# Kernel optimization log

Measured on AMD Instinct MI355X. Metric: run time of the kernel, lower is better.

## Reference

```python
import jax, jax.numpy as jnp
import numpy as np

N_NODES = 250000


def _glorot(key, shape):
    fan_in, fan_out = shape[0], shape[1]
    lim = jnp.sqrt(6.0 / (fan_in + fan_out))
    return jax.random.uniform(key, shape, jnp.float32, -lim, lim)


def setup_inputs() -> dict:
    key = jax.random.key(0)
    ks = jax.random.split(key, 16)
    x = jax.random.normal(ks[0], (N_NODES, 9), jnp.float32)
    edge_index = jax.random.randint(ks[1], (2, 5000000), 0, N_NODES, jnp.int64)
    return {
        "x": x,
        "edge_index": edge_index,
        "W1": _glorot(ks[2], (9, 16)),  "b1": jnp.zeros((16,), jnp.float32),
        "W2": _glorot(ks[3], (16, 16)), "b2": jnp.zeros((16,), jnp.float32),
        "W3": _glorot(ks[4], (16, 16)), "b3": jnp.zeros((16,), jnp.float32),
        "Wl2": _glorot(ks[5], (25, 128)),  "bl2": jnp.zeros((128,), jnp.float32),
        "Wl3": _glorot(ks[6], (128, 128)), "bl3": jnp.zeros((128,), jnp.float32),
        "Wl4": _glorot(ks[7], (128, 1)),   "bl4": jnp.zeros((1,), jnp.float32),
    }


def _gcn_conv(x, src, dst, norm, W, b, n):
    # PyG GCNConv: linear transform, then D^-1/2 (A+I) D^-1/2 aggregation, then bias
    h = x @ W                                   # [N, d_out]
    msg = h[src] * norm[:, None]                # gather + scale   [E+N, d_out]
    agg = jax.ops.segment_sum(msg, dst, num_segments=n)
    return agg + b


def _sym_norm(src, dst, n):
    deg = jax.ops.segment_sum(jnp.ones_like(dst, jnp.float32), dst, num_segments=n)
    dinv = jnp.where(deg > 0, jax.lax.rsqrt(deg), 0.0)
    return dinv[src] * dinv[dst]


def reference(x, edge_index, W1, b1, W2, b2, W3, b3, Wl2, bl2, Wl3, bl3, Wl4, bl4):
    n = x.shape[0]
    loops = jnp.arange(n, dtype=edge_index.dtype)
    src = jnp.concatenate([edge_index[0], loops])  # add self loops
    dst = jnp.concatenate([edge_index[1], loops])
    norm = _sym_norm(src, dst, n)  # same graph for all 3 conv layers

    h = jax.nn.relu(_gcn_conv(x, src, dst, norm, W1, b1, n))
    h = jax.nn.relu(_gcn_conv(h, src, dst, norm, W2, b2, n))
    h = jax.nn.relu(_gcn_conv(h, src, dst, norm, W3, b3, n))

    h = jnp.concatenate([x, h], axis=1)          # [N, 25]
    h = jax.nn.relu(h @ Wl2 + bl2)
    h = jax.nn.relu(h @ Wl3 + bl3)
    return h @ Wl4 + bl4                         # [N, 1]
```

## Files before the change

kernel.cpp:

```cpp
#include <hip/hip_runtime.h>


#define NBLK 512
#define BSH  9
#define BSZ  512
#define MAXNB 1024

__global__ __launch_bounds__(64) void k_detect(const void* __restrict__ edges,
                                               int* __restrict__ flag, int n_nodes)
{
    if (threadIdx.x == 0 && blockIdx.x == 0) {
        const long long* p = (const long long*)edges;
        int is64 = 1;
        for (int i = 0; i < 16; ++i) {
            long long v = p[i];
            if (v < 0 || v >= (long long)n_nodes) is64 = 0;
        }
        *flag = is64;
    }
}

__device__ __forceinline__ int ld_idx(const void* edges, int f64, long long idx)
{
    return f64 ? ((const int*)edges)[idx << 1] : ((const int*)edges)[idx];
}

__global__ __launch_bounds__(256) void k_hist2(const void* __restrict__ edges,
                                               const int* __restrict__ flag,
                                               int* __restrict__ cnt_blk,
                                               long long E, int NB)
{
    __shared__ int cnt[MAXNB];
    int tid = threadIdx.x;
    for (int b = tid; b < NB; b += 256) cnt[b] = 0;
    __syncthreads();
    int f64 = *flag;
    long long chunk = (E + NBLK - 1) / NBLK;
    long long lo = (long long)blockIdx.x * chunk;
    long long hi = lo + chunk; if (hi > E) hi = E;
    for (long long i = lo + tid; i < hi; i += 256) {
        int d = ld_idx(edges, f64, E + i);
        atomicAdd(&cnt[d >> BSH], 1);
    }
    __syncthreads();
    for (int b = tid; b < NB; b += 256)
        cnt_blk[(size_t)b * NBLK + blockIdx.x] = (cnt[b] + 15) & ~15;
}

__global__ __launch_bounds__(256) void k_scan1(const int* __restrict__ in,
                                               int* __restrict__ excl,
                                               int* __restrict__ partials, int n)
{
    __shared__ int s[256];
    int tid = threadIdx.x;
    int i = blockIdx.x * 256 + tid;
    int v = (i < n) ? in[i] : 0;
    s[tid] = v;
    __syncthreads();
#pragma unroll
    for (int off = 1; off < 256; off <<= 1) {
        int t = (tid >= off) ? s[tid - off] : 0;
        __syncthreads();
        s[tid] += t;
        __syncthreads();
    }
    if (i < n) excl[i] = s[tid] - v;
    if (tid == 255) partials[blockIdx.x] = s[255];
}

__global__ __launch_bounds__(1024) void k_scan2(int* __restrict__ p, int nb)
{
    __shared__ int s[1024];
    __shared__ int carry_s;
    int t = threadIdx.x;
    if (t == 0) carry_s = 0;
    __syncthreads();
    for (int base = 0; base < nb; base += 1024) {
        int idx = base + t;
        int v = (idx < nb) ? p[idx] : 0;
        s[t] = v;
        __syncthreads();
        for (int off = 1; off < 1024; off <<= 1) {
            int u = (t >= off) ? s[t - off] : 0;
            __syncthreads();
            s[t] += u;
            __syncthreads();
        }
        int carry = carry_s;
        if (idx < nb) p[idx] = carry + s[t] - v;
        __syncthreads();
        if (t == 0) carry_s += s[1023];
        __syncthreads();
    }
}

__global__ __launch_bounds__(256) void k_scan3(int* __restrict__ excl,
                                               const int* __restrict__ partials, int n)
{
    int i = blockIdx.x * 256 + threadIdx.x;
    if (i < n) excl[i] += partials[blockIdx.x];
}

__global__ __launch_bounds__(256) void k_bin(const void* __restrict__ edges,
                                             const int* __restrict__ flag,
                                             const int* __restrict__ base_blk,
                                             int* __restrict__ epk,
                                             long long E, int NB)
{
    __shared__ int cnt[MAXNB];
    __shared__ int base[MAXNB];
    __shared__ int cur[MAXNB];
    int tid = threadIdx.x;
    for (int b = tid; b < NB; b += 256) cnt[b] = 0;
    __syncthreads();
    int f64 = *flag;
    long long chunk = (E + NBLK - 1) / NBLK;
    long long lo = (long long)blockIdx.x * chunk;
    long long hi = lo + chunk; if (hi > E) hi = E;
    for (long long i = lo + tid; i < hi; i += 256) {
        int d = ld_idx(edges, f64, E + i);
        atomicAdd(&cnt[d >> BSH], 1);
    }
    __syncthreads();
    for (int b = tid; b < NB; b += 256) {
        base[b] = base_blk[(size_t)b * NBLK + blockIdx.x];
        cur[b] = 0;
    }
    __syncthreads();
    for (long long i = lo + tid; i < hi; i += 256) {
        int s = ld_idx(edges, f64, i);
        int d = ld_idx(edges, f64, E + i);
        int b = d >> BSH;
        int slot = atomicAdd(&cur[b], 1);
        epk[base[b] + slot] = ((d & (BSZ - 1)) << 18) | s;
    }
    __syncthreads();
    for (int b = tid; b < NB; b += 256) {
        int c = cnt[b];
        int r = (c + 15) & ~15;
        for (int j = c; j < r; ++j) epk[base[b] + j] = -1;
    }
}

__global__ __launch_bounds__(256) void k_csr(const int* __restrict__ epk,
                                             const int* __restrict__ base_blk,
                                             int* __restrict__ csr,
                                             int* __restrict__ row_off,
                                             int* __restrict__ degi,
                                             float* __restrict__ dinv, int n)
{
    __shared__ int cnt[BSZ];
    __shared__ int off[BSZ];
    __shared__ int ps[256];
    int b = blockIdx.x;
    int tid = threadIdx.x;
    int start = base_blk[(size_t)b * NBLK];
    int end   = base_blk[(size_t)(b + 1) * NBLK];
    cnt[tid] = 0; cnt[tid + 256] = 0;
    __syncthreads();
    for (int e = start + tid; e < end; e += 256) {
        int pk = epk[e];
        if (pk >= 0) atomicAdd(&cnt[pk >> 18], 1);
    }
    __syncthreads();
    int pairSum = cnt[2 * tid] + cnt[2 * tid + 1];
    ps[tid] = pairSum;
    __syncthreads();
#pragma unroll
    for (int o = 1; o < 256; o <<= 1) {
        int v = (tid >= o) ? ps[tid - o] : 0;
        __syncthreads();
        ps[tid] += v;
        __syncthreads();
    }
    int incl = ps[tid];
    off[2 * tid]     = incl - pairSum;
    off[2 * tid + 1] = incl - pairSum + cnt[2 * tid];
    __syncthreads();
    int nbase = b << BSH;
#pragma unroll
    for (int l = tid; l < BSZ; l += 256) {
        int node = nbase + l;
        if (node < n) {
            row_off[node] = start + off[l];
            degi[node]    = cnt[l];
            dinv[node]    = rsqrtf((float)cnt[l] + 1.0f);
        }
    }
    __syncthreads();
    for (int e = start + tid; e < end; e += 256) {
        int pk = epk[e];
        if (pk < 0) continue;
        int l = pk >> 18;
        int pos = atomicAdd(&off[l], 1);
        csr[start + pos] = pk & 0x3FFFF;
    }
}

__global__ __launch_bounds__(256) void k_lin1(const float* __restrict__ x,
                                              const float* __restrict__ W1,
                                              const float* __restrict__ dinv,
                                              float* __restrict__ hs, int n)
{
    __shared__ float sW[144];
    if (threadIdx.x < 144) sW[threadIdx.x] = W1[threadIdx.x];
    __syncthreads();
    int i = blockIdx.x * 256 + threadIdx.x;
    if (i >= n) return;
    float xv[9];
#pragma unroll
    for (int k = 0; k < 9; ++k) xv[k] = x[(size_t)i * 9 + k];
    float di = dinv[i];
#pragma unroll
    for (int j = 0; j < 16; ++j) {
        float acc = 0.f;
#pragma unroll
        for (int k = 0; k < 9; ++k) acc = fmaf(xv[k], sW[k * 16 + j], acc);
        hs[(size_t)i * 16 + j] = acc * di;
    }
}

__global__ __launch_bounds__(256) void k_lin_mid(const float* __restrict__ bias,
                                                 const float* __restrict__ W,
                                                 const float* __restrict__ dinv,
                                                 const float* __restrict__ agg,
                                                 float* __restrict__ hs, int n)
{
    __shared__ float sW[256];
    __shared__ float sB[16];
    sW[threadIdx.x] = W[threadIdx.x];
    if (threadIdx.x < 16) sB[threadIdx.x] = bias[threadIdx.x];
    __syncthreads();
    int i = blockIdx.x * 256 + threadIdx.x;
    if (i >= n) return;
    float t[16];
#pragma unroll
    for (int k = 0; k < 16; ++k) {
        float v = agg[(size_t)i * 16 + k] + sB[k];
        t[k] = v > 0.f ? v : 0.f;
    }
    float di = dinv[i];
#pragma unroll
    for (int j = 0; j < 16; ++j) {
        float acc = 0.f;
#pragma unroll
        for (int k = 0; k < 16; ++k) acc = fmaf(t[k], sW[k * 16 + j], acc);
        hs[(size_t)i * 16 + j] = acc * di;
    }
}

__global__ __launch_bounds__(256) void k_gather(const int* __restrict__ csr,
                                                const int* __restrict__ row_off,
                                                const int* __restrict__ degi,
                                                const float* __restrict__ dinv,
                                                const float* __restrict__ hs,
                                                float* __restrict__ agg, int n)
{
    int wid = (int)(((long long)blockIdx.x * 256 + threadIdx.x) >> 6);
    if (wid >= n) return;
    int lane = threadIdx.x & 63;
    int slot = lane >> 2;
    int q    = lane & 3;
    int start = row_off[wid];
    int deg   = degi[wid];
    float4 sum;
    if (slot == 0) sum = *(const float4*)&hs[(size_t)wid * 16 + q * 4];
    else           sum = make_float4(0.f, 0.f, 0.f, 0.f);
    for (int e = slot; e < deg; e += 16) {
        int s = csr[start + e];
        float4 v = *(const float4*)&hs[(size_t)s * 16 + q * 4];
        sum.x += v.x; sum.y += v.y; sum.z += v.z; sum.w += v.w;
    }
#pragma unroll
    for (int off = 4; off < 64; off <<= 1) {
        sum.x += __shfl_xor(sum.x, off);
        sum.y += __shfl_xor(sum.y, off);
        sum.z += __shfl_xor(sum.z, off);
        sum.w += __shfl_xor(sum.w, off);
    }
    if (slot == 0) {
        float di = dinv[wid];
        sum.x *= di; sum.y *= di; sum.z *= di; sum.w *= di;
        *(float4*)&agg[(size_t)wid * 16 + q * 4] = sum;
    }
}

__global__ __launch_bounds__(256) void k_mlp(const float* __restrict__ x,
                                             const float* __restrict__ agg3,
                                             const float* __restrict__ b3,
                                             const float* __restrict__ Wl2,
                                             const float* __restrict__ bl2,
                                             const float* __restrict__ Wl3,
                                             const float* __restrict__ bl3,
                                             const float* __restrict__ Wl4,
                                             const float* __restrict__ bl4,
                                             float* __restrict__ out, int n)
{
    __shared__ __align__(16) float zs[4][16][132];
    __shared__ __align__(16) float sfeat[4][16][28];

    int tid  = threadIdx.x;
    int w    = tid >> 6;
    int lane = tid & 63;
    int og   = lane & 15;
    int ng   = lane >> 4;
    int base = (blockIdx.x * 4 + w) * 16;

    for (int idx = lane; idx < 16 * 25; idx += 64) {
        int nn = idx / 25, f = idx - nn * 25;
        int node = base + nn;
        float v = 0.f;
        if (node < n) {
            if (f < 9) v = x[(size_t)node * 9 + f];
            else {
                float t = agg3[(size_t)node * 16 + (f - 9)] + b3[f - 9];
                v = t > 0.f ? t : 0.f;
            }
        }
        sfeat[w][nn][f] = v;
    }
    __syncthreads();

    float acc[4][8];
    {
        float4 b0 = *(const float4*)&bl2[og * 8];
        float4 b1 = *(const float4*)&bl2[og * 8 + 4];
#pragma unroll
        for (int i = 0; i < 4; ++i) {
            acc[i][0] = b0.x; acc[i][1] = b0.y; acc[i][2] = b0.z; acc[i][3] = b0.w;
            acc[i][4] = b1.x; acc[i][5] = b1.y; acc[i][6] = b1.z; acc[i][7] = b1.w;
        }
    }
#pragma unroll
    for (int k = 0; k < 25; ++k) {
        float4 w0 = *(const float4*)&Wl2[k * 128 + og * 8];
        float4 w1 = *(const float4*)&Wl2[k * 128 + og * 8 + 4];
#pragma unroll
        for (int i = 0; i < 4; ++i) {
            float f = sfeat[w][ng * 4 + i][k];
            acc[i][0] = fmaf(f, w0.x, acc[i][0]); acc[i][1] = fmaf(f, w0.y, acc[i][1]);
            acc[i][2] = fmaf(f, w0.z, acc[i][2]); acc[i][3] = fmaf(f, w0.w, acc[i][3]);
            acc[i][4] = fmaf(f, w1.x, acc[i][4]); acc[i][5] = fmaf(f, w1.y, acc[i][5]);
            acc[i][6] = fmaf(f, w1.z, acc[i][6]); acc[i][7] = fmaf(f, w1.w, acc[i][7]);
        }
    }
#pragma unroll
    for (int i = 0; i < 4; ++i) {
        float4 lo, hi;
        lo.x = acc[i][0] > 0.f ? acc[i][0] : 0.f; lo.y = acc[i][1] > 0.f ? acc[i][1] : 0.f;
        lo.z = acc[i][2] > 0.f ? acc[i][2] : 0.f; lo.w = acc[i][3] > 0.f ? acc[i][3] : 0.f;
        hi.x = acc[i][4] > 0.f ? acc[i][4] : 0.f; hi.y = acc[i][5] > 0.f ? acc[i][5] : 0.f;
        hi.z = acc[i][6] > 0.f ? acc[i][6] : 0.f; hi.w = acc[i][7] > 0.f ? acc[i][7] : 0.f;
        *(float4*)&zs[w][ng * 4 + i][og * 8]     = lo;
        *(float4*)&zs[w][ng * 4 + i][og * 8 + 4] = hi;
    }
    __syncthreads();

    {
        float4 b0 = *(const float4*)&bl3[og * 8];
        float4 b1 = *(const float4*)&bl3[og * 8 + 4];
#pragma unroll
        for (int i = 0; i < 4; ++i) {
            acc[i][0] = b0.x; acc[i][1] = b0.y; acc[i][2] = b0.z; acc[i][3] = b0.w;
            acc[i][4] = b1.x; acc[i][5] = b1.y; acc[i][6] = b1.z; acc[i][7] = b1.w;
        }
    }
#pragma unroll 2
    for (int k4 = 0; k4 < 64; k4 += 4) {
        float4 z4[4];
#pragma unroll
        for (int i = 0; i < 4; ++i)
            z4[i] = *(const float4*)&zs[w][ng * 4 + i][k4];
#pragma unroll
        for (int kk = 0; kk < 4; ++kk) {
            const float* wr = &Wl3[(k4 + kk) * 128 + og * 8];
            float4 w0 = *(const float4*)wr;
            float4 w1 = *(const float4*)(wr + 4);
#pragma unroll
            for (int i = 0; i < 4; ++i) {
                float zz = (kk == 0) ? z4[i].x : (kk == 1) ? z4[i].y
                         : (kk == 2) ? z4[i].z : z4[i].w;
                acc[i][0] = fmaf(zz, w0.x, acc[i][0]); acc[i][1] = fmaf(zz, w0.y, acc[i][1]);
                acc[i][2] = fmaf(zz, w0.z, acc[i][2]); acc[i][3] = fmaf(zz, w0.w, acc[i][3]);
                acc[i][4] = fmaf(zz, w1.x, acc[i][4]); acc[i][5] = fmaf(zz, w1.y, acc[i][5]);
                acc[i][6] = fmaf(zz, w1.z, acc[i][6]); acc[i][7] = fmaf(zz, w1.w, acc[i][7]);
            }
        }
    }
    __syncthreads();
#pragma unroll 2
    for (int k4 = 64; k4 < 128; k4 += 4) {
        float4 z4[4];
#pragma unroll
        for (int i = 0; i < 4; ++i)
            z4[i] = *(const float4*)&zs[w][ng * 4 + i][k4];
#pragma unroll
        for (int kk = 0; kk < 4; ++kk) {
            const float* wr = &Wl3[(k4 + kk) * 128 + og * 8];
            float4 w0 = *(const float4*)wr;
            float4 w1 = *(const float4*)(wr + 4);
#pragma unroll
            for (int i = 0; i < 4; ++i) {
                float zz = (kk == 0) ? z4[i].x : (kk == 1) ? z4[i].y
                         : (kk == 2) ? z4[i].z : z4[i].w;
                acc[i][0] = fmaf(zz, w0.x, acc[i][0]); acc[i][1] = fmaf(zz, w0.y, acc[i][1]);
                acc[i][2] = fmaf(zz, w0.z, acc[i][2]); acc[i][3] = fmaf(zz, w0.w, acc[i][3]);
                acc[i][4] = fmaf(zz, w1.x, acc[i][4]); acc[i][5] = fmaf(zz, w1.y, acc[i][5]);
                acc[i][6] = fmaf(zz, w1.z, acc[i][6]); acc[i][7] = fmaf(zz, w1.w, acc[i][7]);
            }
        }
    }

    {
        float4 w40 = *(const float4*)&Wl4[og * 8];
        float4 w41 = *(const float4*)&Wl4[og * 8 + 4];
        float bb = bl4[0];
#pragma unroll
        for (int i = 0; i < 4; ++i) {
            float p = 0.f;
            p = fmaf(acc[i][0] > 0.f ? acc[i][0] : 0.f, w40.x, p);
            p = fmaf(acc[i][1] > 0.f ? acc[i][1] : 0.f, w40.y, p);
            p = fmaf(acc[i][2] > 0.f ? acc[i][2] : 0.f, w40.z, p);
            p = fmaf(acc[i][3] > 0.f ? acc[i][3] : 0.f, w40.w, p);
            p = fmaf(acc[i][4] > 0.f ? acc[i][4] : 0.f, w41.x, p);
            p = fmaf(acc[i][5] > 0.f ? acc[i][5] : 0.f, w41.y, p);
            p = fmaf(acc[i][6] > 0.f ? acc[i][6] : 0.f, w41.z, p);
            p = fmaf(acc[i][7] > 0.f ? acc[i][7] : 0.f, w41.w, p);
            p += __shfl_xor(p, 1);
            p += __shfl_xor(p, 2);
            p += __shfl_xor(p, 4);
            p += __shfl_xor(p, 8);
            int node = base + ng * 4 + i;
            if (og == 0 && node < n) out[node] = p + bb;
        }
    }
}

extern "C" void kernel_launch(void* const* d_in, const int* in_sizes, int n_in,
                              void* d_out, int out_size, void* d_ws, size_t ws_size,
                              hipStream_t stream)
{
    const float* x   = (const float*)d_in[0];
    const void*  ei  = d_in[1];
    const float* W1  = (const float*)d_in[2];
    const float* b1  = (const float*)d_in[3];
    const float* W2  = (const float*)d_in[4];
    const float* b2  = (const float*)d_in[5];
    const float* W3  = (const float*)d_in[6];
    const float* b3  = (const float*)d_in[7];
    const float* Wl2 = (const float*)d_in[8];
    const float* bl2 = (const float*)d_in[9];
    const float* Wl3 = (const float*)d_in[10];
    const float* bl3 = (const float*)d_in[11];
    const float* Wl4 = (const float*)d_in[12];
    const float* bl4 = (const float*)d_in[13];
    float* out = (float*)d_out;

    int n        = in_sizes[0] / 9;
    long long e2 = (long long)in_sizes[1];
    long long E  = e2 / 2;
    int NB       = (n + BSZ - 1) >> BSH;
    int L        = NB * NBLK + 1;
    size_t EPAD  = (size_t)E + (size_t)NBLK * NB * 16;

    char* ws = (char*)d_ws;
    size_t off = 0;
    int*   flag     = (int*)(ws + off); off += 256;
    int*   cnt_blk  = (int*)(ws + off); off += (size_t)L * 4;        off = (off + 255) & ~(size_t)255;
    int*   base_blk = (int*)(ws + off); off += (size_t)L * 4;        off = (off + 255) & ~(size_t)255;
    int*   partials = (int*)(ws + off); off += 16384;
    float* dinv     = (float*)(ws + off); off += (size_t)n * 4;      off = (off + 255) & ~(size_t)255;
    int*   degi     = (int*)(ws + off); off += (size_t)n * 4;        off = (off + 255) & ~(size_t)255;
    int*   row_off  = (int*)(ws + off); off += (size_t)n * 4;        off = (off + 255) & ~(size_t)255;
    int*   csr      = (int*)(ws + off); off += EPAD * 4;             off = (off + 255) & ~(size_t)255;
    int*   epk      = (int*)(ws + off); off += EPAD * 4;             off = (off + 255) & ~(size_t)255;
    float* hs  = (float*)epk;
    float* agg = hs + (size_t)n * 16;

    int nb_n = (n + 255) / 256;
    int nb_s = (L + 255) / 256;

    k_detect<<<1, 64, 0, stream>>>(ei, flag, n);
    hipMemsetAsync(cnt_blk + (L - 1), 0, 4, stream);
    k_hist2<<<NBLK, 256, 0, stream>>>(ei, flag, cnt_blk, E, NB);
    k_scan1<<<nb_s, 256, 0, stream>>>(cnt_blk, base_blk, partials, L);
    k_scan2<<<1, 1024, 0, stream>>>(partials, nb_s);
    k_scan3<<<nb_s, 256, 0, stream>>>(base_blk, partials, L);
    k_bin<<<NBLK, 256, 0, stream>>>(ei, flag, base_blk, epk, E, NB);
    k_csr<<<NB, 256, 0, stream>>>(epk, base_blk, csr, row_off, degi, dinv, n);

    int nb_g = (n + 3) / 4;
    k_lin1<<<nb_n, 256, 0, stream>>>(x, W1, dinv, hs, n);
    k_gather<<<nb_g, 256, 0, stream>>>(csr, row_off, degi, dinv, hs, agg, n);
    k_lin_mid<<<nb_n, 256, 0, stream>>>(b1, W2, dinv, agg, hs, n);
    k_gather<<<nb_g, 256, 0, stream>>>(csr, row_off, degi, dinv, hs, agg, n);
    k_lin_mid<<<nb_n, 256, 0, stream>>>(b2, W3, dinv, agg, hs, n);
    k_gather<<<nb_g, 256, 0, stream>>>(csr, row_off, degi, dinv, hs, agg, n);
    k_mlp<<<(n + 63) / 64, 256, 0, stream>>>(x, agg, b3, Wl2, bl2, Wl3, bl3, Wl4, bl4,
                                             out, n);
}
```

Measured before the change: 602.7 us.

## Fuse GCN linear transform into gather kernel and swizzle MLP shared memory

Merges the per-node 16x16 linear transform (bias, ReLU, matmul, dinv scale) into the neighbor-gather kernel, so the two middle k_lin_mid launches and their round trip of the aggregate buffer through global memory go away. Gather and transform now ping-pong between two buffers. The gather loop is unrolled by two to keep more independent loads in flight. The MLP kernel reuses one shared buffer for both input features and hidden activations, and uses an XOR swizzle instead of padding to avoid bank conflicts, which lowers shared memory use but adds an extra barrier.

```diff
diff --git a/kernel.cpp b/kernel.cpp
--- a/kernel.cpp
+++ b/kernel.cpp
@@ -220,41 +220,15 @@
     }
 }
 
-__global__ __launch_bounds__(256) void k_lin_mid(const float* __restrict__ bias,
+template<int MODE>
+__global__ __launch_bounds__(256) void k_gatherF(const int* __restrict__ csr,
+                                                 const int* __restrict__ row_off,
+                                                 const int* __restrict__ degi,
+                                                 const float* __restrict__ dinv,
+                                                 const float* __restrict__ hs,
                                                  const float* __restrict__ W,
-                                                 const float* __restrict__ dinv,
-                                                 const float* __restrict__ agg,
-                                                 float* __restrict__ hs, int n)
-{
-    __shared__ float sW[256];
-    __shared__ float sB[16];
-    sW[threadIdx.x] = W[threadIdx.x];
-    if (threadIdx.x < 16) sB[threadIdx.x] = bias[threadIdx.x];
-    __syncthreads();
-    int i = blockIdx.x * 256 + threadIdx.x;
-    if (i >= n) return;
-    float t[16];
-#pragma unroll
-    for (int k = 0; k < 16; ++k) {
-        float v = agg[(size_t)i * 16 + k] + sB[k];
-        t[k] = v > 0.f ? v : 0.f;
-    }
-    float di = dinv[i];
-#pragma unroll
-    for (int j = 0; j < 16; ++j) {
-        float acc = 0.f;
-#pragma unroll
-        for (int k = 0; k < 16; ++k) acc = fmaf(t[k], sW[k * 16 + j], acc);
-        hs[(size_t)i * 16 + j] = acc * di;
-    }
-}
-
-__global__ __launch_bounds__(256) void k_gather(const int* __restrict__ csr,
-                                                const int* __restrict__ row_off,
-                                                const int* __restrict__ degi,
-                                                const float* __restrict__ dinv,
-                                                const float* __restrict__ hs,
-                                                float* __restrict__ agg, int n)
+                                                 const float* __restrict__ bias,
+                                                 float* __restrict__ outb, int n)
 {
     int wid = (int)(((long long)blockIdx.x * 256 + threadIdx.x) >> 6);
     if (wid >= n) return;
@@ -263,13 +237,23 @@
     int q    = lane & 3;
     int start = row_off[wid];
     int deg   = degi[wid];
+    float di  = dinv[wid];
     float4 sum;
     if (slot == 0) sum = *(const float4*)&hs[(size_t)wid * 16 + q * 4];
     else           sum = make_float4(0.f, 0.f, 0.f, 0.f);
-    for (int e = slot; e < deg; e += 16) {
-        int s = csr[start + e];
-        float4 v = *(const float4*)&hs[(size_t)s * 16 + q * 4];
-        sum.x += v.x; sum.y += v.y; sum.z += v.z; sum.w += v.w;
+    int e = slot;
+    for (; e + 16 < deg; e += 32) {
+        int s0 = csr[start + e];
+        int s1 = csr[start + e + 16];
+        float4 v0 = *(const float4*)&hs[(size_t)s0 * 16 + q * 4];
+        float4 v1 = *(const float4*)&hs[(size_t)s1 * 16 + q * 4];
+        sum.x += v0.x + v1.x; sum.y += v0.y + v1.y;
+        sum.z += v0.z + v1.z; sum.w += v0.w + v1.w;
+    }
+    if (e < deg) {
+        int s0 = csr[start + e];
+        float4 v0 = *(const float4*)&hs[(size_t)s0 * 16 + q * 4];
+        sum.x += v0.x; sum.y += v0.y; sum.z += v0.z; sum.w += v0.w;
     }
 #pragma unroll
     for (int off = 4; off < 64; off <<= 1) {
@@ -278,10 +262,30 @@
         sum.z += __shfl_xor(sum.z, off);
         sum.w += __shfl_xor(sum.w, off);
     }
-    if (slot == 0) {
-        float di = dinv[wid];
-        sum.x *= di; sum.y *= di; sum.z *= di; sum.w *= di;
-        *(float4*)&agg[(size_t)wid * 16 + q * 4] = sum;
+    float4 aq = make_float4(sum.x * di, sum.y * di, sum.z * di, sum.w * di);
+
+    if (MODE == 0) {
+        if (slot == 0) *(float4*)&outb[(size_t)wid * 16 + q * 4] = aq;
+    } else {
+        float t[16];
+#pragma unroll
+        for (int a = 0; a < 4; ++a) {
+            t[4 * a + 0] = __shfl(aq.x, a);
+            t[4 * a + 1] = __shfl(aq.y, a);
+            t[4 * a + 2] = __shfl(aq.z, a);
+            t[4 * a + 3] = __shfl(aq.w, a);
+        }
+#pragma unroll
+        for (int k = 0; k < 16; ++k) {
+            float v = t[k] + bias[k];
+            t[k] = v > 0.f ? v : 0.f;
+        }
+        int j = lane & 15;
+        float o = 0.f;
+#pragma unroll
+        for (int k = 0; k < 16; ++k)
+            o = fmaf(t[k], W[k * 16 + j], o);
+        if (lane < 16) outb[(size_t)wid * 16 + j] = o * di;
     }
 }
 
@@ -296,8 +300,7 @@
                                              const float* __restrict__ bl4,
                                              float* __restrict__ out, int n)
 {
-    __shared__ __align__(16) float zs[4][16][132];
-    __shared__ __align__(16) float sfeat[4][16][28];
+    __shared__ __align__(16) float zs[4][16][128];
 
     int tid  = threadIdx.x;
     int w    = tid >> 6;
@@ -317,7 +320,7 @@
                 v = t > 0.f ? t : 0.f;
             }
         }
-        sfeat[w][nn][f] = v;
+        zs[w][nn][f] = v;
     }
     __syncthreads();
 
@@ -337,22 +340,26 @@
         float4 w1 = *(const float4*)&Wl2[k * 128 + og * 8 + 4];
 #pragma unroll
         for (int i = 0; i < 4; ++i) {
-            float f = sfeat[w][ng * 4 + i][k];
+            float f = zs[w][ng * 4 + i][k];
             acc[i][0] = fmaf(f, w0.x, acc[i][0]); acc[i][1] = fmaf(f, w0.y, acc[i][1]);
             acc[i][2] = fmaf(f, w0.z, acc[i][2]); acc[i][3] = fmaf(f, w0.w, acc[i][3]);
             acc[i][4] = fmaf(f, w1.x, acc[i][4]); acc[i][5] = fmaf(f, w1.y, acc[i][5]);
             acc[i][6] = fmaf(f, w1.z, acc[i][6]); acc[i][7] = fmaf(f, w1.w, acc[i][7]);
         }
     }
-#pragma unroll
-    for (int i = 0; i < 4; ++i) {
-        float4 lo, hi;
-        lo.x = acc[i][0] > 0.f ? acc[i][0] : 0.f; lo.y = acc[i][1] > 0.f ? acc[i][1] : 0.f;
-        lo.z = acc[i][2] > 0.f ? acc[i][2] : 0.f; lo.w = acc[i][3] > 0.f ? acc[i][3] : 0.f;
-        hi.x = acc[i][4] > 0.f ? acc[i][4] : 0.f; hi.y = acc[i][5] > 0.f ? acc[i][5] : 0.f;
-        hi.z = acc[i][6] > 0.f ? acc[i][6] : 0.f; hi.w = acc[i][7] > 0.f ? acc[i][7] : 0.f;
-        *(float4*)&zs[w][ng * 4 + i][og * 8]     = lo;
-        *(float4*)&zs[w][ng * 4 + i][og * 8 + 4] = hi;
+    __syncthreads();
+    {
+        int c0 = (og * 8) ^ (ng << 3);
+#pragma unroll
+        for (int i = 0; i < 4; ++i) {
+            float4 lo, hi;
+            lo.x = acc[i][0] > 0.f ? acc[i][0] : 0.f; lo.y = acc[i][1] > 0.f ? acc[i][1] : 0.f;
+            lo.z = acc[i][2] > 0.f ? acc[i][2] : 0.f; lo.w = acc[i][3] > 0.f ? acc[i][3] : 0.f;
+            hi.x = acc[i][4] > 0.f ? acc[i][4] : 0.f; hi.y = acc[i][5] > 0.f ? acc[i][5] : 0.f;
+            hi.z = acc[i][6] > 0.f ? acc[i][6] : 0.f; hi.w = acc[i][7] > 0.f ? acc[i][7] : 0.f;
+            *(float4*)&zs[w][ng * 4 + i][c0]     = lo;
+            *(float4*)&zs[w][ng * 4 + i][c0 + 4] = hi;
+        }
     }
     __syncthreads();
 
@@ -365,12 +372,13 @@
             acc[i][4] = b1.x; acc[i][5] = b1.y; acc[i][6] = b1.z; acc[i][7] = b1.w;
         }
     }
+    int swz = ng << 3;
 #pragma unroll 2
     for (int k4 = 0; k4 < 64; k4 += 4) {
         float4 z4[4];
 #pragma unroll
         for (int i = 0; i < 4; ++i)
-            z4[i] = *(const float4*)&zs[w][ng * 4 + i][k4];
+            z4[i] = *(const float4*)&zs[w][ng * 4 + i][k4 ^ swz];
 #pragma unroll
         for (int kk = 0; kk < 4; ++kk) {
             const float* wr = &Wl3[(k4 + kk) * 128 + og * 8];
@@ -393,7 +401,7 @@
         float4 z4[4];
 #pragma unroll
         for (int i = 0; i < 4; ++i)
-            z4[i] = *(const float4*)&zs[w][ng * 4 + i][k4];
+            z4[i] = *(const float4*)&zs[w][ng * 4 + i][k4 ^ swz];
 #pragma unroll
         for (int kk = 0; kk < 4; ++kk) {
             const float* wr = &Wl3[(k4 + kk) * 128 + og * 8];
@@ -474,8 +482,8 @@
     int*   row_off  = (int*)(ws + off); off += (size_t)n * 4;        off = (off + 255) & ~(size_t)255;
     int*   csr      = (int*)(ws + off); off += EPAD * 4;             off = (off + 255) & ~(size_t)255;
     int*   epk      = (int*)(ws + off); off += EPAD * 4;             off = (off + 255) & ~(size_t)255;
-    float* hs  = (float*)epk;
-    float* agg = hs + (size_t)n * 16;
+    float* bufA = (float*)epk;
+    float* bufB = bufA + (size_t)n * 16;
 
     int nb_n = (n + 255) / 256;
     int nb_s = (L + 255) / 256;
@@ -490,12 +498,13 @@
     k_csr<<<NB, 256, 0, stream>>>(epk, base_blk, csr, row_off, degi, dinv, n);
 
     int nb_g = (n + 3) / 4;
-    k_lin1<<<nb_n, 256, 0, stream>>>(x, W1, dinv, hs, n);
-    k_gather<<<nb_g, 256, 0, stream>>>(csr, row_off, degi, dinv, hs, agg, n);
-    k_lin_mid<<<nb_n, 256, 0, stream>>>(b1, W2, dinv, agg, hs, n);
-    k_gather<<<nb_g, 256, 0, stream>>>(csr, row_off, degi, dinv, hs, agg, n);
-    k_lin_mid<<<nb_n, 256, 0, stream>>>(b2, W3, dinv, agg, hs, n);
-    k_gather<<<nb_g, 256, 0, stream>>>(csr, row_off, degi, dinv, hs, agg, n);
-    k_mlp<<<(n + 63) / 64, 256, 0, stream>>>(x, agg, b3, Wl2, bl2, Wl3, bl3, Wl4, bl4,
+    k_lin1<<<nb_n, 256, 0, stream>>>(x, W1, dinv, bufA, n);
+    k_gatherF<1><<<nb_g, 256, 0, stream>>>(csr, row_off, degi, dinv, bufA, W2, b1,
+                                           bufB, n);
+    k_gatherF<1><<<nb_g, 256, 0, stream>>>(csr, row_off, degi, dinv, bufB, W3, b2,
+                                           bufA, n);
+    k_gatherF<0><<<nb_g, 256, 0, stream>>>(csr, row_off, degi, dinv, bufA, nullptr,
+                                           nullptr, bufB, n);
+    k_mlp<<<(n + 63) / 64, 256, 0, stream>>>(x, bufB, b3, Wl2, bl2, Wl3, bl3, Wl4, bl4,
                                              out, n);
 }
```

After: 593.3 us. No clear change (-1.6%).
